# Kernel tuning notes

Measured on AMD Instinct MI355X. Metric: run time of the kernel, lower is better.

The kernel has to match this reference:

```python
import jax, jax.numpy as jnp
import numpy as np
import math

D = 1024
H = 16
C = D // H
EPS = 1e-5

def layernorm(x, g, b):
    mu = jnp.mean(x, axis=-1, keepdims=True)
    var = jnp.mean(jnp.square(x - mu), axis=-1, keepdims=True)
    return (x - mu) * jax.lax.rsqrt(var + EPS) * g + b

def setup_inputs() -> dict:
    key = jax.random.key(0)
    ks = jax.random.split(key, 12)
    s = 1.0 / math.sqrt(D)
    inp = {
        "x": jax.random.normal(ks[0], (4, 2048, D), dtype=jnp.float32),
        "src_mask": jnp.ones((4, 2048), dtype=bool),
        "Wk": jax.random.normal(ks[1], (D, D), dtype=jnp.float32) * s,
        "Wq": jax.random.normal(ks[2], (D, D), dtype=jnp.float32) * s,
        "Wv": jax.random.normal(ks[3], (D, D), dtype=jnp.float32) * s,
        "Wfc": jax.random.normal(ks[4], (D, D), dtype=jnp.float32) * s,
        "bfc": jnp.zeros((D,), dtype=jnp.float32),
        "g1": jnp.ones((D,), dtype=jnp.float32),
        "b1": jnp.zeros((D,), dtype=jnp.float32),
        "g2": jnp.ones((D,), dtype=jnp.float32),
        "b2": jnp.zeros((D,), dtype=jnp.float32),
        "W1": jax.random.normal(ks[5], (D, 4 * D), dtype=jnp.float32) * s,
        "bf1": jnp.zeros((4 * D,), dtype=jnp.float32),
        "W2": jax.random.normal(ks[6], (4 * D, D), dtype=jnp.float32) * (1.0 / math.sqrt(4 * D)),
        "bf2": jnp.zeros((D,), dtype=jnp.float32),
    }
    return inp

def reference(x, src_mask, Wk, Wq, Wv, Wfc, bfc, g1, b1, g2, b2, W1, bf1, W2, bf2):
    b, s, _ = x.shape
    xl = layernorm(x, g1, b1)
    # self-attention (src_mask is unused in the original module)
    k = (xl @ Wk).reshape(b, s, H, C).transpose(0, 2, 1, 3)  # bhsc
    q = (xl @ Wq).reshape(b, s, H, C).transpose(0, 2, 1, 3)
    v = (xl @ Wv).reshape(b, s, H, C).transpose(0, 2, 1, 3)
    # NOTE: original multiplies by sqrt(c) (not divide) -- faithful quirk
    scores = jnp.einsum('bhqc,bhkc->bhqk', q, k) * math.sqrt(C)
    attn = jax.nn.softmax(scores, axis=-1)
    o = jnp.einsum('bhqk,bhkc->bhqc', attn, v)
    o = o.transpose(0, 2, 1, 3).reshape(b, s, D)
    ka = o @ Wfc + bfc
    x = ka + x
    xl2 = layernorm(x, g2, b2)
    ff = jax.nn.relu(xl2 @ W1 + bf1) @ W2 + bf2
    return ff + x
```

## Files before the change

kernel.cpp:

```cpp
#include <hip/hip_runtime.h>
#include <hip/hip_bf16.h>
#include <math.h>


typedef __hip_bfloat16 bf16_t;
typedef __bf16 bf16x8 __attribute__((ext_vector_type(8)));
typedef float f32x4 __attribute__((ext_vector_type(4)));

#define LN_EPS 1e-5f
#define QSCALE 11.541560327111707f

__device__ __forceinline__ void async_copy16(const bf16_t* g, bf16_t* l) {
  __builtin_amdgcn_global_load_lds(
      (const __attribute__((address_space(1))) void*)g,
      (__attribute__((address_space(3))) void*)l,
      16 , 0 , 0 );
}

__device__ __forceinline__ void split_bf16(float v, bf16_t& hi, bf16_t& lo) {
  hi = __float2bfloat16(v);
  lo = __float2bfloat16(v - __bfloat162float(hi));
}

template<bool SPLIT>
__global__ __launch_bounds__(256) void ln_kernel(
    const float* __restrict__ x, const float* __restrict__ g,
    const float* __restrict__ b, bf16_t* __restrict__ out_hi,
    bf16_t* __restrict__ out_lo)
{
  const int row = blockIdx.x;
  const int tid = threadIdx.x;
  const float4 v = *(const float4*)(x + (size_t)row * 1024 + tid * 4);
  float s  = v.x + v.y + v.z + v.w;
  float ss = v.x * v.x + v.y * v.y + v.z * v.z + v.w * v.w;
  for (int off = 32; off > 0; off >>= 1) {
    s  += __shfl_down(s, off);
    ss += __shfl_down(ss, off);
  }
  __shared__ float sb[4], ssb[4];
  const int wave = tid >> 6, lane = tid & 63;
  if (lane == 0) { sb[wave] = s; ssb[wave] = ss; }
  __syncthreads();
  const float tot  = sb[0] + sb[1] + sb[2] + sb[3];
  const float tots = ssb[0] + ssb[1] + ssb[2] + ssb[3];
  const float mu   = tot * (1.0f / 1024.0f);
  const float var  = tots * (1.0f / 1024.0f) - mu * mu;
  const float rstd = rsqrtf(var + LN_EPS);
  const float4 gv = *(const float4*)(g + tid * 4);
  const float4 bv = *(const float4*)(b + tid * 4);
  float y[4] = {(v.x - mu) * rstd * gv.x + bv.x,
                (v.y - mu) * rstd * gv.y + bv.y,
                (v.z - mu) * rstd * gv.z + bv.z,
                (v.w - mu) * rstd * gv.w + bv.w};
  bf16_t hi[4] __attribute__((aligned(8)));
  bf16_t lo[4] __attribute__((aligned(8)));
  #pragma unroll
  for (int i = 0; i < 4; i++) split_bf16(y[i], hi[i], lo[i]);
  uint2 ph, pl;
  __builtin_memcpy(&ph, hi, 8);
  *(uint2*)(out_hi + (size_t)row * 1024 + tid * 4) = ph;
  if (SPLIT) {
    __builtin_memcpy(&pl, lo, 8);
    *(uint2*)(out_lo + (size_t)row * 1024 + tid * 4) = pl;
  }
}

__global__ __launch_bounds__(256) void wtrans_all_kernel(
    const float* __restrict__ Wq, const float* __restrict__ Wk,
    const float* __restrict__ Wv, const float* __restrict__ Wfc,
    const float* __restrict__ W1, const float* __restrict__ W2,
    bf16_t* __restrict__ WqkH, bf16_t* __restrict__ WqkL,
    bf16_t* __restrict__ WvT, bf16_t* __restrict__ WfcT,
    bf16_t* __restrict__ W1T, bf16_t* __restrict__ W2T)
{
  const int id = blockIdx.x;
  const float* W; bf16_t* DH; bf16_t* DL = nullptr;
  int K, N, n0, k0;
  if (id < 4096) {
    K = 1024; N = 1024;
    const int local = id & 1023;
    n0 = (local & 31) * 32; k0 = (local >> 5) * 32;
    if (id < 1024)      { W = Wq;  DH = WqkH;                 DL = WqkL; }
    else if (id < 2048) { W = Wk;  DH = WqkH + 1024 * 1024;   DL = WqkL + 1024 * 1024; }
    else if (id < 3072) { W = Wv;  DH = WvT; }
    else                { W = Wfc; DH = WfcT; }
  } else if (id < 8192) {
    const int local = id - 4096;
    K = 1024; N = 4096; W = W1; DH = W1T;
    n0 = (local & 127) * 32; k0 = (local >> 7) * 32;
  } else {
    const int local = id - 8192;
    K = 4096; N = 1024; W = W2; DH = W2T;
    n0 = (local & 31) * 32; k0 = (local >> 5) * 32;
  }
  __shared__ float t[32][33];
  const int tx = threadIdx.x & 31, ty = threadIdx.x >> 5;
  #pragma unroll
  for (int r = ty; r < 32; r += 8)
    t[r][tx] = W[(size_t)(k0 + r) * N + n0 + tx];
  __syncthreads();
  #pragma unroll
  for (int r = ty; r < 32; r += 8) {
    const float v = t[tx][r];
    bf16_t hi, lo;
    split_bf16(v, hi, lo);
    DH[(size_t)(n0 + r) * K + k0 + tx] = hi;
    if (DL) DL[(size_t)(n0 + r) * K + k0 + tx] = lo;
  }
}

template<bool BIAS, bool RELU, bool RESID, bool OUTBF>
__global__ __launch_bounds__(256) void gemm_kernel(
    const bf16_t* __restrict__ A, const bf16_t* __restrict__ BT,
    const float* __restrict__ bias, const float* __restrict__ resid,
    float* __restrict__ outF, bf16_t* __restrict__ outB,
    int M, int N, int K)
{
  __shared__ __align__(16) bf16_t As[128 * 64];
  __shared__ __align__(16) bf16_t Bs[128 * 64];
  const int nblk = N >> 7;
  const int bm = blockIdx.x / nblk;
  const int bn = blockIdx.x % nblk;
  const int tid  = threadIdx.x;
  const int wave = tid >> 6;
  const int lane = tid & 63;
  const int l15  = lane & 15;
  const int quad = lane >> 4;
  const int wm = wave >> 1, wn = wave & 1;

  const int srow = lane >> 3;
  const int schunk = (lane & 7) ^ srow;
  const bf16_t* aG = A  + (size_t)(bm * 128 + wave * 32 + srow) * K + schunk * 8;
  const bf16_t* bG = BT + (size_t)(bn * 128 + wave * 32 + srow) * K + schunk * 8;

  f32x4 acc[4][4];
  #pragma unroll
  for (int i = 0; i < 4; i++)
    #pragma unroll
    for (int j = 0; j < 4; j++) acc[i][j] = (f32x4){0.f, 0.f, 0.f, 0.f};

  const int rsw = l15 & 7;

  for (int kt = 0; kt < K; kt += 64) {
    #pragma unroll
    for (int j = 0; j < 4; j++) {
      async_copy16(aG + kt + (size_t)(j * 8) * K, &As[(wave * 32 + j * 8) * 64]);
      async_copy16(bG + kt + (size_t)(j * 8) * K, &Bs[(wave * 32 + j * 8) * 64]);
    }
    __syncthreads();
    #pragma unroll
    for (int ko = 0; ko < 2; ko++) {
      bf16x8 af[4], bfr[4];
      #pragma unroll
      for (int i = 0; i < 4; i++)
        af[i]  = *(const bf16x8*)&As[(wm * 64 + i * 16 + l15) * 64 +
                                     (((ko * 4 + quad) ^ rsw) * 8)];
      #pragma unroll
      for (int j = 0; j < 4; j++)
        bfr[j] = *(const bf16x8*)&Bs[(wn * 64 + j * 16 + l15) * 64 +
                                     (((ko * 4 + quad) ^ rsw) * 8)];
      #pragma unroll
      for (int i = 0; i < 4; i++)
        #pragma unroll
        for (int j = 0; j < 4; j++)
          acc[i][j] = __builtin_amdgcn_mfma_f32_16x16x32_bf16(af[i], bfr[j], acc[i][j], 0, 0, 0);
    }
    __syncthreads();
  }

  const int gm0 = bm * 128 + wm * 64 + quad * 4;
  const int gn0 = bn * 128 + wn * 64 + l15;
  #pragma unroll
  for (int i = 0; i < 4; i++) {
    #pragma unroll
    for (int j = 0; j < 4; j++) {
      const int gn = gn0 + j * 16;
      const float bz = BIAS ? bias[gn] : 0.0f;
      #pragma unroll
      for (int r = 0; r < 4; r++) {
        const int gm = gm0 + i * 16 + r;
        float v = acc[i][j][r] + bz;
        if (RESID) v += resid[(size_t)gm * N + gn];
        if (RELU)  v = fmaxf(v, 0.0f);
        if (OUTBF) outB[(size_t)gm * N + gn] = __float2bfloat16(v);
        else       outF[(size_t)gm * N + gn] = v;
      }
    }
  }
}

__global__ __launch_bounds__(256) void gemm_split_kernel(
    const bf16_t* __restrict__ Ah, const bf16_t* __restrict__ Al,
    const bf16_t* __restrict__ Bh, const bf16_t* __restrict__ Bl,
    bf16_t* __restrict__ out_hi, bf16_t* __restrict__ out_lo,
    int M, int N, int K)
{
  __shared__ __align__(16) bf16_t AsH[128 * 32];
  __shared__ __align__(16) bf16_t AsL[128 * 32];
  __shared__ __align__(16) bf16_t BsH[128 * 32];
  __shared__ __align__(16) bf16_t BsL[128 * 32];
  const int nblk = N >> 7;
  const int bm = blockIdx.x / nblk;
  const int bn = blockIdx.x % nblk;
  const int tid  = threadIdx.x;
  const int wave = tid >> 6;
  const int lane = tid & 63;
  const int l15  = lane & 15;
  const int quad = lane >> 4;
  const int wm = wave >> 1, wn = wave & 1;

  const int srow = lane >> 2;
  const int schunk = (lane & 3) ^ ((lane >> 3) & 3);
  const size_t aOff = (size_t)(bm * 128 + wave * 32 + srow) * K + schunk * 8;
  const size_t bOff = (size_t)(bn * 128 + wave * 32 + srow) * K + schunk * 8;
  const int ldsOff0 = (wave * 32) * 32;
  const int ldsOff1 = (wave * 32 + 16) * 32;

  f32x4 acc[4][4];
  #pragma unroll
  for (int i = 0; i < 4; i++)
    #pragma unroll
    for (int j = 0; j < 4; j++) acc[i][j] = (f32x4){0.f, 0.f, 0.f, 0.f};

  const int rsw = (l15 >> 1) & 3;

  for (int kt = 0; kt < K; kt += 32) {
    async_copy16(Ah + aOff + kt, &AsH[ldsOff0]);
    async_copy16(Ah + aOff + kt + (size_t)16 * K, &AsH[ldsOff1]);
    async_copy16(Al + aOff + kt, &AsL[ldsOff0]);
    async_copy16(Al + aOff + kt + (size_t)16 * K, &AsL[ldsOff1]);
    async_copy16(Bh + bOff + kt, &BsH[ldsOff0]);
    async_copy16(Bh + bOff + kt + (size_t)16 * K, &BsH[ldsOff1]);
    async_copy16(Bl + bOff + kt, &BsL[ldsOff0]);
    async_copy16(Bl + bOff + kt + (size_t)16 * K, &BsL[ldsOff1]);
    __syncthreads();
    bf16x8 afH[4], afL[4], bfH[4], bfL[4];
    #pragma unroll
    for (int i = 0; i < 4; i++) {
      const int o = (wm * 64 + i * 16 + l15) * 32 + ((quad ^ rsw) * 8);
      afH[i] = *(const bf16x8*)&AsH[o];
      afL[i] = *(const bf16x8*)&AsL[o];
    }
    #pragma unroll
    for (int j = 0; j < 4; j++) {
      const int o = (wn * 64 + j * 16 + l15) * 32 + ((quad ^ rsw) * 8);
      bfH[j] = *(const bf16x8*)&BsH[o];
      bfL[j] = *(const bf16x8*)&BsL[o];
    }
    #pragma unroll
    for (int i = 0; i < 4; i++)
      #pragma unroll
      for (int j = 0; j < 4; j++) {
        acc[i][j] = __builtin_amdgcn_mfma_f32_16x16x32_bf16(afH[i], bfH[j], acc[i][j], 0, 0, 0);
        acc[i][j] = __builtin_amdgcn_mfma_f32_16x16x32_bf16(afH[i], bfL[j], acc[i][j], 0, 0, 0);
        acc[i][j] = __builtin_amdgcn_mfma_f32_16x16x32_bf16(afL[i], bfH[j], acc[i][j], 0, 0, 0);
      }
    __syncthreads();
  }

  const int gm0 = bm * 128 + wm * 64 + quad * 4;
  const int gn0 = bn * 128 + wn * 64 + l15;
  #pragma unroll
  for (int i = 0; i < 4; i++)
    #pragma unroll
    for (int j = 0; j < 4; j++) {
      const int gn = gn0 + j * 16;
      const float scale = (gn < 1024) ? QSCALE : 1.0f;
      #pragma unroll
      for (int r = 0; r < 4; r++) {
        const int gm = gm0 + i * 16 + r;
        bf16_t hi, lo;
        split_bf16(acc[i][j][r] * scale, hi, lo);
        out_hi[(size_t)gm * N + gn] = hi;
        out_lo[(size_t)gm * N + gn] = lo;
      }
    }
}

__global__ __launch_bounds__(256) void attn_kernel(
    const bf16_t* __restrict__ qkH,
    const bf16_t* __restrict__ qkL,
    const bf16_t* __restrict__ vT,
    bf16_t* __restrict__ o)
{
  const int qt = blockIdx.x;
  const int h  = blockIdx.y;
  const int b  = blockIdx.z;
  const int wave = threadIdx.x >> 6;
  const int lane = threadIdx.x & 63;
  const int l15  = lane & 15;
  const int quad = lane >> 4;
  const int sw   = l15 & 7;
  const int qrowA = qt * 128 + wave * 32;
  const int qrowB = qrowA + 16;

  __shared__ __align__(16) bf16_t SMEM[20480];
  bf16_t* Kbig = SMEM;
  bf16_t* KhL  = SMEM;
  bf16_t* KlL  = SMEM + 4096;
  bf16_t* VtL  = SMEM + 8192;
  bf16_t* pw   = SMEM + 12288 + wave * 2048;

  const size_t tok0 = (size_t)b * 2048;
  const size_t qoffA = (tok0 + qrowA + l15) * 2048 + h * 64;
  const size_t qoffB = (tok0 + qrowB + l15) * 2048 + h * 64;
  const bf16x8 aA0H = *(const bf16x8*)(qkH + qoffA + quad * 8);
  const bf16x8 aA1H = *(const bf16x8*)(qkH + qoffA + 32 + quad * 8);
  const bf16x8 aA0L = *(const bf16x8*)(qkL + qoffA + quad * 8);
  const bf16x8 aA1L = *(const bf16x8*)(qkL + qoffA + 32 + quad * 8);
  const bf16x8 aB0H = *(const bf16x8*)(qkH + qoffB + quad * 8);
  const bf16x8 aB1H = *(const bf16x8*)(qkH + qoffB + 32 + quad * 8);
  const bf16x8 aB0L = *(const bf16x8*)(qkL + qoffB + quad * 8);
  const bf16x8 aB1L = *(const bf16x8*)(qkL + qoffB + 32 + quad * 8);

  const int kOff = 1024 + h * 64;
  const int rsub = lane >> 3;
  const int csw  = (lane & 7) ^ (rsub & 7);

  f32x4 mxA = (f32x4){-3.0e38f, -3.0e38f, -3.0e38f, -3.0e38f};
  f32x4 mxB = mxA;
  for (int kb = 0; kb < 2048; kb += 256) {
    #pragma unroll
    for (int j = 0; j < 8; j++) {
      const int row0 = wave * 64 + j * 8;
      async_copy16(qkH + (tok0 + kb + row0 + rsub) * 2048 + kOff + csw * 8,
                   &Kbig[row0 * 64]);
    }
    __syncthreads();
    #pragma unroll
    for (int t = 0; t < 16; t++) {
      const int base = (t * 16 + l15) * 64;
      const bf16x8 bh0 = *(const bf16x8*)&Kbig[base + ((quad) ^ sw) * 8];
      const bf16x8 bh1 = *(const bf16x8*)&Kbig[base + ((4 + quad) ^ sw) * 8];
      f32x4 accA = (f32x4){0.f, 0.f, 0.f, 0.f};
      f32x4 accB = accA;
      accA = __builtin_amdgcn_mfma_f32_16x16x32_bf16(aA0H, bh0, accA, 0, 0, 0);
      accA = __builtin_amdgcn_mfma_f32_16x16x32_bf16(aA1H, bh1, accA, 0, 0, 0);
      accB = __builtin_amdgcn_mfma_f32_16x16x32_bf16(aB0H, bh0, accB, 0, 0, 0);
      accB = __builtin_amdgcn_mfma_f32_16x16x32_bf16(aB1H, bh1, accB, 0, 0, 0);
      #pragma unroll
      for (int r = 0; r < 4; r++) {
        mxA[r] = fmaxf(mxA[r], accA[r]);
        mxB[r] = fmaxf(mxB[r], accB[r]);
      }
    }
    __syncthreads();
  }
  f32x4 negMA, negMB;
  #pragma unroll
  for (int r = 0; r < 4; r++) {
    float mA = mxA[r], mB = mxB[r];
    mA = fmaxf(mA, __shfl_xor(mA, 1)); mB = fmaxf(mB, __shfl_xor(mB, 1));
    mA = fmaxf(mA, __shfl_xor(mA, 2)); mB = fmaxf(mB, __shfl_xor(mB, 2));
    mA = fmaxf(mA, __shfl_xor(mA, 4)); mB = fmaxf(mB, __shfl_xor(mB, 4));
    mA = fmaxf(mA, __shfl_xor(mA, 8)); mB = fmaxf(mB, __shfl_xor(mB, 8));
    negMA[r] = -(mA + 4.0f);
    negMB[r] = -(mB + 4.0f);
  }

  f32x4 OfA[4], OfB[4];
  f32x4 lsumA = (f32x4){0.f, 0.f, 0.f, 0.f};
  f32x4 lsumB = lsumA;
  #pragma unroll
  for (int c = 0; c < 4; c++) { OfA[c] = lsumA; OfB[c] = lsumA; }

  for (int kb = 0; kb < 2048; kb += 64) {
    #pragma unroll
    for (int j = 0; j < 2; j++) {
      const int row0 = wave * 16 + j * 8;
      const size_t krow = tok0 + kb + row0 + rsub;
      async_copy16(qkH + krow * 2048 + kOff + csw * 8, &KhL[row0 * 64]);
      async_copy16(qkL + krow * 2048 + kOff + csw * 8, &KlL[row0 * 64]);
      async_copy16(vT + (size_t)(h * 64 + row0 + rsub) * 8192 + tok0 + kb + csw * 8,
                   &VtL[row0 * 64]);
    }
    __syncthreads();

    #pragma unroll
    for (int t = 0; t < 4; t++) {
      const int base = (t * 16 + l15) * 64;
      const bf16x8 bh0 = *(const bf16x8*)&KhL[base + ((quad) ^ sw) * 8];
      const bf16x8 bh1 = *(const bf16x8*)&KhL[base + ((4 + quad) ^ sw) * 8];
      const bf16x8 bl0 = *(const bf16x8*)&KlL[base + ((quad) ^ sw) * 8];
      const bf16x8 bl1 = *(const bf16x8*)&KlL[base + ((4 + quad) ^ sw) * 8];
      f32x4 accA = negMA;
      f32x4 accB = negMB;
      accA = __builtin_amdgcn_mfma_f32_16x16x32_bf16(aA0H, bh0, accA, 0, 0, 0);
      accA = __builtin_amdgcn_mfma_f32_16x16x32_bf16(aA1H, bh1, accA, 0, 0, 0);
      accA = __builtin_amdgcn_mfma_f32_16x16x32_bf16(aA0H, bl0, accA, 0, 0, 0);
      accA = __builtin_amdgcn_mfma_f32_16x16x32_bf16(aA1H, bl1, accA, 0, 0, 0);
      accA = __builtin_amdgcn_mfma_f32_16x16x32_bf16(aA0L, bh0, accA, 0, 0, 0);
      accA = __builtin_amdgcn_mfma_f32_16x16x32_bf16(aA1L, bh1, accA, 0, 0, 0);
      accB = __builtin_amdgcn_mfma_f32_16x16x32_bf16(aB0H, bh0, accB, 0, 0, 0);
      accB = __builtin_amdgcn_mfma_f32_16x16x32_bf16(aB1H, bh1, accB, 0, 0, 0);
      accB = __builtin_amdgcn_mfma_f32_16x16x32_bf16(aB0H, bl0, accB, 0, 0, 0);
      accB = __builtin_amdgcn_mfma_f32_16x16x32_bf16(aB1H, bl1, accB, 0, 0, 0);
      accB = __builtin_amdgcn_mfma_f32_16x16x32_bf16(aB0L, bh0, accB, 0, 0, 0);
      accB = __builtin_amdgcn_mfma_f32_16x16x32_bf16(aB1L, bh1, accB, 0, 0, 0);
      #pragma unroll
      for (int r = 0; r < 4; r++) {
        const float pA = __builtin_amdgcn_exp2f(accA[r]);
        const float pB = __builtin_amdgcn_exp2f(accB[r]);
        lsumA[r] += pA;
        lsumB[r] += pB;
        const int RA = quad * 4 + r;
        const int RB = 16 + RA;
        pw[RA * 64 + (((t * 2 + (l15 >> 3)) ^ (RA & 7)) * 8) + (l15 & 7)] =
            __float2bfloat16(pA);
        pw[RB * 64 + (((t * 2 + (l15 >> 3)) ^ (RB & 7)) * 8) + (l15 & 7)] =
            __float2bfloat16(pB);
      }
    }

    const bf16x8 paA0 = *(const bf16x8*)&pw[l15 * 64 + ((quad) ^ sw) * 8];
    const bf16x8 paA1 = *(const bf16x8*)&pw[l15 * 64 + ((4 + quad) ^ sw) * 8];
    const bf16x8 paB0 = *(const bf16x8*)&pw[(16 + l15) * 64 + ((quad) ^ sw) * 8];
    const bf16x8 paB1 = *(const bf16x8*)&pw[(16 + l15) * 64 + ((4 + quad) ^ sw) * 8];
    #pragma unroll
    for (int c = 0; c < 4; c++) {
      const int vb = (c * 16 + l15) * 64;
      const bf16x8 bv0 = *(const bf16x8*)&VtL[vb + ((quad) ^ sw) * 8];
      const bf16x8 bv1 = *(const bf16x8*)&VtL[vb + ((4 + quad) ^ sw) * 8];
      OfA[c] = __builtin_amdgcn_mfma_f32_16x16x32_bf16(paA0, bv0, OfA[c], 0, 0, 0);
      OfA[c] = __builtin_amdgcn_mfma_f32_16x16x32_bf16(paA1, bv1, OfA[c], 0, 0, 0);
      OfB[c] = __builtin_amdgcn_mfma_f32_16x16x32_bf16(paB0, bv0, OfB[c], 0, 0, 0);
      OfB[c] = __builtin_amdgcn_mfma_f32_16x16x32_bf16(paB1, bv1, OfB[c], 0, 0, 0);
    }
    __syncthreads();
  }

  float lrowA[4], lrowB[4];
  #pragma unroll
  for (int r = 0; r < 4; r++) {
    float cA = lsumA[r], cB = lsumB[r];
    cA += __shfl_xor(cA, 1); cB += __shfl_xor(cB, 1);
    cA += __shfl_xor(cA, 2); cB += __shfl_xor(cB, 2);
    cA += __shfl_xor(cA, 4); cB += __shfl_xor(cB, 4);
    cA += __shfl_xor(cA, 8); cB += __shfl_xor(cB, 8);
    lrowA[r] = cA; lrowB[r] = cB;
  }

  bf16_t* opA = o + (tok0 + qrowA) * 1024 + h * 64;
  bf16_t* opB = o + (tok0 + qrowB) * 1024 + h * 64;
  #pragma unroll
  for (int c = 0; c < 4; c++)
    #pragma unroll
    for (int r = 0; r < 4; r++) {
      opA[(size_t)(quad * 4 + r) * 1024 + c * 16 + l15] =
          __float2bfloat16(OfA[c][r] / lrowA[r]);
      opB[(size_t)(quad * 4 + r) * 1024 + c * 16 + l15] =
          __float2bfloat16(OfB[c][r] / lrowB[r]);
    }
}

extern "C" void kernel_launch(void* const* d_in, const int* in_sizes, int n_in,
                              void* d_out, int out_size, void* d_ws, size_t ws_size,
                              hipStream_t stream)
{
  (void)in_sizes; (void)n_in; (void)out_size; (void)ws_size;
  const float* x   = (const float*)d_in[0];
  const float* Wk  = (const float*)d_in[2];
  const float* Wq  = (const float*)d_in[3];
  const float* Wv  = (const float*)d_in[4];
  const float* Wfc = (const float*)d_in[5];
  const float* bfc = (const float*)d_in[6];
  const float* g1  = (const float*)d_in[7];
  const float* b1  = (const float*)d_in[8];
  const float* g2  = (const float*)d_in[9];
  const float* b2  = (const float*)d_in[10];
  const float* W1  = (const float*)d_in[11];
  const float* bf1 = (const float*)d_in[12];
  const float* W2  = (const float*)d_in[13];
  const float* bf2 = (const float*)d_in[14];
  float* out = (float*)d_out;

  char* ws = (char*)d_ws;
  bf16_t* xl_hi  = (bf16_t*)(ws + (0ull   << 20));
  bf16_t* oAtt   = xl_hi;
  bf16_t* xl_lo  = (bf16_t*)(ws + (16ull  << 20));
  bf16_t* vT     = xl_lo;
  bf16_t* xl2    = xl_lo;
  bf16_t* qk_hi  = (bf16_t*)(ws + (32ull  << 20));
  bf16_t* qk_lo  = (bf16_t*)(ws + (64ull  << 20));
  bf16_t* h1     = qk_hi;
  float*  x2     = (float*) (ws + (112ull << 20));
  bf16_t* Wqk_hi = (bf16_t*)(ws + (144ull << 20));
  bf16_t* Wqk_lo = (bf16_t*)(ws + (148ull << 20));
  bf16_t* WvT    = (bf16_t*)(ws + (152ull << 20));
  bf16_t* WfcT   = (bf16_t*)(ws + (154ull << 20));
  bf16_t* W1T    = (bf16_t*)(ws + (156ull << 20));
  bf16_t* W2T    = (bf16_t*)(ws + (164ull << 20));

  const dim3 blk(256);

  wtrans_all_kernel<<<12288, blk, 0, stream>>>(
      Wq, Wk, Wv, Wfc, W1, W2, Wqk_hi, Wqk_lo, WvT, WfcT, W1T, W2T);

  ln_kernel<true><<<8192, blk, 0, stream>>>(x, g1, b1, xl_hi, xl_lo);

  gemm_split_kernel<<<64 * 16, blk, 0, stream>>>(
      xl_hi, xl_lo, Wqk_hi, Wqk_lo, qk_hi, qk_lo, 8192, 2048, 1024);

  gemm_kernel<false, false, false, true><<<8 * 64, blk, 0, stream>>>(
      WvT, xl_hi, nullptr, nullptr, nullptr, vT, 1024, 8192, 1024);

  attn_kernel<<<dim3(16, 16, 4), blk, 0, stream>>>(qk_hi, qk_lo, vT, oAtt);

  gemm_kernel<true, false, true, false><<<64 * 8, blk, 0, stream>>>(
      oAtt, WfcT, bfc, x, x2, nullptr, 8192, 1024, 1024);

  ln_kernel<false><<<8192, blk, 0, stream>>>(x2, g2, b2, xl2, nullptr);

  gemm_kernel<true, true, false, true><<<64 * 32, blk, 0, stream>>>(
      xl2, W1T, bf1, nullptr, nullptr, h1, 8192, 4096, 1024);

  gemm_kernel<true, false, true, false><<<64 * 8, blk, 0, stream>>>(
      h1, W2T, bf2, x2, out, nullptr, 8192, 1024, 4096);
}
```

Measured before the change: 669.8 us.

## Replace two-pass max pre-scan with lazy online-softmax rescaling in attention

Removes the separate first pass over all keys that computed row maxima. The running max now starts at zero and is rescaled only when a tile's scores exceed a threshold; when that happens, the lsum, the output accumulators and the already-written P entries in LDS are scaled down. This saves one full pass of K loads and MFMAs per query tile, at the cost of a wave-uniform branch per subtile and occasional rescale work that adds extra bf16 rounding of stored probabilities.

```diff
diff --git a/kernel.cpp b/kernel.cpp
--- a/kernel.cpp
+++ b/kernel.cpp
@@ -9,6 +9,7 @@
 
 #define LN_EPS 1e-5f
 #define QSCALE 11.541560327111707f
+#define RESCALE_THR 8.0f
 
 __device__ __forceinline__ void async_copy16(const bf16_t* g, bf16_t* l) {
   __builtin_amdgcn_global_load_lds(
@@ -295,7 +296,6 @@
   const int qrowB = qrowA + 16;
 
   __shared__ __align__(16) bf16_t SMEM[20480];
-  bf16_t* Kbig = SMEM;
   bf16_t* KhL  = SMEM;
   bf16_t* KlL  = SMEM + 4096;
   bf16_t* VtL  = SMEM + 8192;
@@ -317,47 +317,8 @@
   const int rsub = lane >> 3;
   const int csw  = (lane & 7) ^ (rsub & 7);
 
-  f32x4 mxA = (f32x4){-3.0e38f, -3.0e38f, -3.0e38f, -3.0e38f};
-  f32x4 mxB = mxA;
-  for (int kb = 0; kb < 2048; kb += 256) {
-    #pragma unroll
-    for (int j = 0; j < 8; j++) {
-      const int row0 = wave * 64 + j * 8;
-      async_copy16(qkH + (tok0 + kb + row0 + rsub) * 2048 + kOff + csw * 8,
-                   &Kbig[row0 * 64]);
-    }
-    __syncthreads();
-    #pragma unroll
-    for (int t = 0; t < 16; t++) {
-      const int base = (t * 16 + l15) * 64;
-      const bf16x8 bh0 = *(const bf16x8*)&Kbig[base + ((quad) ^ sw) * 8];
-      const bf16x8 bh1 = *(const bf16x8*)&Kbig[base + ((4 + quad) ^ sw) * 8];
-      f32x4 accA = (f32x4){0.f, 0.f, 0.f, 0.f};
-      f32x4 accB = accA;
-      accA = __builtin_amdgcn_mfma_f32_16x16x32_bf16(aA0H, bh0, accA, 0, 0, 0);
-      accA = __builtin_amdgcn_mfma_f32_16x16x32_bf16(aA1H, bh1, accA, 0, 0, 0);
-      accB = __builtin_amdgcn_mfma_f32_16x16x32_bf16(aB0H, bh0, accB, 0, 0, 0);
-      accB = __builtin_amdgcn_mfma_f32_16x16x32_bf16(aB1H, bh1, accB, 0, 0, 0);
-      #pragma unroll
-      for (int r = 0; r < 4; r++) {
-        mxA[r] = fmaxf(mxA[r], accA[r]);
-        mxB[r] = fmaxf(mxB[r], accB[r]);
-      }
-    }
-    __syncthreads();
-  }
-  f32x4 negMA, negMB;
-  #pragma unroll
-  for (int r = 0; r < 4; r++) {
-    float mA = mxA[r], mB = mxB[r];
-    mA = fmaxf(mA, __shfl_xor(mA, 1)); mB = fmaxf(mB, __shfl_xor(mB, 1));
-    mA = fmaxf(mA, __shfl_xor(mA, 2)); mB = fmaxf(mB, __shfl_xor(mB, 2));
-    mA = fmaxf(mA, __shfl_xor(mA, 4)); mB = fmaxf(mB, __shfl_xor(mB, 4));
-    mA = fmaxf(mA, __shfl_xor(mA, 8)); mB = fmaxf(mB, __shfl_xor(mB, 8));
-    negMA[r] = -(mA + 4.0f);
-    negMB[r] = -(mB + 4.0f);
-  }
-
+  f32x4 negMA = (f32x4){0.f, 0.f, 0.f, 0.f};
+  f32x4 negMB = negMA;
   f32x4 OfA[4], OfB[4];
   f32x4 lsumA = (f32x4){0.f, 0.f, 0.f, 0.f};
   f32x4 lsumB = lsumA;
@@ -397,6 +358,38 @@
       accB = __builtin_amdgcn_mfma_f32_16x16x32_bf16(aB1H, bl1, accB, 0, 0, 0);
       accB = __builtin_amdgcn_mfma_f32_16x16x32_bf16(aB0L, bh0, accB, 0, 0, 0);
       accB = __builtin_amdgcn_mfma_f32_16x16x32_bf16(aB1L, bh1, accB, 0, 0, 0);
+
+      float pmax = fmaxf(fmaxf(fmaxf(accA[0], accA[1]), fmaxf(accA[2], accA[3])),
+                         fmaxf(fmaxf(accB[0], accB[1]), fmaxf(accB[2], accB[3])));
+      if (!__all(pmax <= RESCALE_THR)) {
+        #pragma unroll
+        for (int r = 0; r < 4; r++) {
+          float mA = accA[r], mB = accB[r];
+          mA = fmaxf(mA, __shfl_xor(mA, 1)); mB = fmaxf(mB, __shfl_xor(mB, 1));
+          mA = fmaxf(mA, __shfl_xor(mA, 2)); mB = fmaxf(mB, __shfl_xor(mB, 2));
+          mA = fmaxf(mA, __shfl_xor(mA, 4)); mB = fmaxf(mB, __shfl_xor(mB, 4));
+          mA = fmaxf(mA, __shfl_xor(mA, 8)); mB = fmaxf(mB, __shfl_xor(mB, 8));
+          const float sA = fmaxf(mA, 0.0f);
+          const float sB = fmaxf(mB, 0.0f);
+          const float fA = __builtin_amdgcn_exp2f(-sA);
+          const float fB = __builtin_amdgcn_exp2f(-sB);
+          negMA[r] -= sA;  negMB[r] -= sB;
+          lsumA[r] *= fA;  lsumB[r] *= fB;
+          #pragma unroll
+          for (int c = 0; c < 4; c++) { OfA[c][r] *= fA; OfB[c][r] *= fB; }
+          accA[r] -= sA;   accB[r] -= sB;
+          const int RA = quad * 4 + r;
+          const int RB = 16 + RA;
+          #pragma unroll
+          for (int tp = 0; tp < t; tp++) {
+            const int iA = RA * 64 + (((tp * 2 + (l15 >> 3)) ^ (RA & 7)) * 8) + (l15 & 7);
+            const int iB = RB * 64 + (((tp * 2 + (l15 >> 3)) ^ (RB & 7)) * 8) + (l15 & 7);
+            pw[iA] = __float2bfloat16(__bfloat162float(pw[iA]) * fA);
+            pw[iB] = __float2bfloat16(__bfloat162float(pw[iB]) * fB);
+          }
+        }
+      }
+
       #pragma unroll
       for (int r = 0; r < 4; r++) {
         const float pA = __builtin_amdgcn_exp2f(accA[r]);
```

After: 837.7 us. +25.1%, slower.
